# Performance work log

Hardware: AMD Instinct MI355X
Metric: run time of the kernel (lower is better)

## Reference

```python
import jax, jax.numpy as jnp
import numpy as np

DIM = 1024
N_HEADS = 16
B, S = 2, 2048


def setup_inputs() -> dict:
    key = jax.random.key(0)
    ks = jax.random.split(key, 5)
    scale = 1.0 / np.sqrt(DIM)
    x = jax.random.normal(ks[0], (B, S, DIM), dtype=jnp.float32)
    mask = jax.random.randint(ks[1], (B, S), 0, 2, dtype=jnp.int32)
    Wq = jax.random.normal(ks[2], (DIM, DIM), dtype=jnp.float32) * scale
    Wk = jax.random.normal(ks[3], (DIM, DIM), dtype=jnp.float32) * scale
    Wv = jax.random.normal(ks[4], (DIM, DIM), dtype=jnp.float32) * scale
    bq = jnp.zeros((DIM,), jnp.float32)
    bk = jnp.zeros((DIM,), jnp.float32)
    bv = jnp.zeros((DIM,), jnp.float32)
    return {"x": x, "mask": mask, "Wq": Wq, "bq": bq, "Wk": Wk, "bk": bk, "Wv": Wv, "bv": bv}


def reference(x, mask, Wq, bq, Wk, bk, Wv, bv):
    # x: (B,S,D); project to q,k,v then split heads: (B,H,S,Dh)
    H = N_HEADS
    Bn, Sn, D = x.shape
    Dh = D // H

    def heads(t):
        return t.reshape(Bn, Sn, H, Dh).transpose(0, 2, 1, 3)

    q = heads(x @ Wq + bq)
    k = heads(x @ Wk + bk)
    v = heads(x @ Wv + bv)

    scores = jnp.einsum("bhsd,bhtd->bhst", q, k) / jnp.sqrt(jnp.float32(Dh))
    m = mask.astype(jnp.float32)[:, None, None, :]  # (B,1,1,S)
    scores = scores - 10000.0 * (1.0 - m)
    attn = jax.nn.softmax(scores, axis=-1)  # dropout is identity at eval (p=0)
    h = jnp.einsum("bhst,bhtd->bhsd", attn, v)
    return h.transpose(0, 2, 1, 3).reshape(Bn, Sn, D)
```

## Files before the change

### kernel.cpp

```cpp
#include <hip/hip_runtime.h>
#include <math.h>

#define DIMD 1024
#define NH 16
#define DH 64
#define BB 2
#define SS 2048
#define M_TOTAL (BB * SS)

typedef _Float16 half8 __attribute__((ext_vector_type(8)));
typedef _Float16 half4v __attribute__((ext_vector_type(4)));
typedef __fp16 fp16x2 __attribute__((ext_vector_type(2)));
typedef float floatx4 __attribute__((ext_vector_type(4)));
typedef float floatx16 __attribute__((ext_vector_type(16)));

#define QSCALE 0.18033688011112042f

__device__ __forceinline__ void load16_to_lds(const void* g, void* l) {
    __builtin_amdgcn_global_load_lds(
        (const __attribute__((address_space(1))) void*)g,
        (__attribute__((address_space(3))) void*)l, 16, 0, 0);
}

__global__ __launch_bounds__(256) void prep_kernel(
    const float* __restrict__ x,
    const float* __restrict__ Wq, const float* __restrict__ Wk,
    const float* __restrict__ Wv, const int* __restrict__ mask,
    _Float16* __restrict__ xh, _Float16* __restrict__ Wt,
    int* __restrict__ pos, int* __restrict__ nvalid)
{
    __shared__ _Float16 Ls[32][34];
    __shared__ int cnt[32], off[32];
    const int bid = blockIdx.x, tid = threadIdx.x;

    if (bid < 1024) {
#pragma unroll
        for (int j = 0; j < 4; ++j) {
            const int i = j * 262144 + bid * 256 + tid;
            float4 v = ((const float4*)x)[i];
            half4v hv = {(_Float16)v.x, (_Float16)v.y, (_Float16)v.z, (_Float16)v.w};
            *(half4v*)&xh[(size_t)i * 4] = hv;
        }
    } else if (bid < 4096) {
        const int wid = bid - 1024;
        const int z = wid >> 10, rem = wid & 1023;
        const float* W = z == 0 ? Wq : (z == 1 ? Wk : Wv);
        _Float16* o = Wt + (size_t)z * DIMD * DIMD;
        const int k0 = (rem >> 5) * 32, n0 = (rem & 31) * 32;
        const int r = tid >> 3, c4 = (tid & 7) * 4;

        float4 v = *(const float4*)&W[(size_t)(k0 + r) * DIMD + n0 + c4];
        Ls[r][c4 + 0] = (_Float16)v.x;
        Ls[r][c4 + 1] = (_Float16)v.y;
        Ls[r][c4 + 2] = (_Float16)v.z;
        Ls[r][c4 + 3] = (_Float16)v.w;
        __syncthreads();
        half4v h = {Ls[c4 + 0][r], Ls[c4 + 1][r], Ls[c4 + 2][r], Ls[c4 + 3][r]};
        *(half4v*)&o[(size_t)(n0 + r) * DIMD + k0 + c4] = h;
    } else {
        const int b = bid - 4096;
        const int wv = tid >> 6, lane = tid & 63;
        const unsigned long long lanemask = (lane == 63)
            ? 0x7fffffffffffffffull : ((1ull << lane) - 1ull);
        unsigned long long bms[8];
#pragma unroll
        for (int cc = 0; cc < 8; ++cc) {
            const int c = wv * 8 + cc;
            const int mv = mask[b * SS + c * 64 + lane];
            bms[cc] = __ballot(mv != 0);
            if (lane == 0) cnt[c] = __popcll(bms[cc]);
        }
        __syncthreads();
        if (tid == 0) {
            int s = 0;
            for (int c = 0; c < 32; ++c) { off[c] = s; s += cnt[c]; }
            nvalid[b] = s;
        }
        __syncthreads();
#pragma unroll
        for (int cc = 0; cc < 8; ++cc) {
            const int c = wv * 8 + cc;
            const int valid = (int)((bms[cc] >> lane) & 1ull);
            pos[b * SS + c * 64 + lane] =
                valid ? (off[c] + __popcll(bms[cc] & lanemask)) : -1;
        }
    }
}

__global__ __launch_bounds__(256) void proj_gemm(
    const _Float16* __restrict__ xh, const _Float16* __restrict__ Wt,
    const float* __restrict__ bq, const float* __restrict__ bk,
    const float* __restrict__ bv, const int* __restrict__ pos,
    _Float16* __restrict__ Q, _Float16* __restrict__ K, _Float16* __restrict__ Vt)
{
    const int z = blockIdx.z;
    const float* bias = z == 0 ? bq : (z == 1 ? bk : bv);
    const _Float16* Wz = Wt + (size_t)z * DIMD * DIMD;

    const _Float16* Aptr; const _Float16* Bptr; int m0, n0;
    if (z == 2) { Aptr = Wz; Bptr = xh; m0 = blockIdx.y * 128; n0 = blockIdx.x * 128; }
    else        { Aptr = xh; Bptr = Wz; m0 = blockIdx.x * 128; n0 = blockIdx.y * 128; }

    __shared__ _Float16 Ah[2][128 * 32];
    __shared__ _Float16 Bh[2][128 * 32];

    const int tid = threadIdx.x;
    const int wave = tid >> 6, lane = tid & 63;
    const int quad = lane >> 4, l16 = lane & 15;
    const int wm = (wave >> 1) * 64, wn = (wave & 1) * 64;

    floatx4 acc[4][4];
#pragma unroll
    for (int i = 0; i < 4; ++i)
#pragma unroll
        for (int j = 0; j < 4; ++j) acc[i][j] = (floatx4){0.f, 0.f, 0.f, 0.f};

    auto stage = [&](int buf, int k0) {
#pragma unroll
        for (int it = 0; it < 2; ++it) {
            const int u = it * 256 + tid;
            const int row = u >> 2;
            const int gc = (u & 3) ^ ((row >> 1) & 3);
            load16_to_lds(&Aptr[(size_t)(m0 + row) * DIMD + k0 + gc * 8],
                          &Ah[buf][(size_t)(it * 256 + wave * 64) * 8]);
        }
#pragma unroll
        for (int it = 0; it < 2; ++it) {
            const int u = it * 256 + tid;
            const int row = u >> 2;
            const int gc = (u & 3) ^ ((row >> 1) & 3);
            load16_to_lds(&Bptr[(size_t)(n0 + row) * DIMD + k0 + gc * 8],
                          &Bh[buf][(size_t)(it * 256 + wave * 64) * 8]);
        }
    };

    stage(0, 0);
    __syncthreads();

    for (int kt = 0; kt < 32; ++kt) {
        if (kt + 1 < 32) stage((kt + 1) & 1, (kt + 1) * 32);

        const _Float16* A = Ah[kt & 1];
        const _Float16* B = Bh[kt & 1];
        half8 af[4], bf[4];
#pragma unroll
        for (int mt = 0; mt < 4; ++mt) {
            const int row = wm + mt * 16 + l16;
            af[mt] = *(const half8*)&A[row * 32 + ((quad ^ ((row >> 1) & 3)) << 3)];
        }
#pragma unroll
        for (int nt = 0; nt < 4; ++nt) {
            const int row = wn + nt * 16 + l16;
            bf[nt] = *(const half8*)&B[row * 32 + ((quad ^ ((row >> 1) & 3)) << 3)];
        }
#pragma unroll
        for (int mt = 0; mt < 4; ++mt)
#pragma unroll
            for (int nt = 0; nt < 4; ++nt)
                acc[mt][nt] = __builtin_amdgcn_mfma_f32_16x16x32_f16(
                    af[mt], bf[nt], acc[mt][nt], 0, 0, 0);

        __syncthreads();
    }

    if (z < 2) {
        int prr[4][4];
#pragma unroll
        for (int mt = 0; mt < 4; ++mt)
#pragma unroll
            for (int r = 0; r < 4; ++r) {
                const int m = m0 + wm + mt * 16 + quad * 4 + r;
                prr[mt][r] = (z == 0) ? (m & 2047) : pos[m];
            }
#pragma unroll
        for (int nt = 0; nt < 4; ++nt) {
            const int n = n0 + wn + nt * 16 + l16;
            const float bn = bias[n];
            const int h = n >> 6, d = n & 63;
#pragma unroll
            for (int mt = 0; mt < 4; ++mt) {
#pragma unroll
                for (int r = 0; r < 4; ++r) {
                    if (prr[mt][r] < 0) continue;
                    const int m = m0 + wm + mt * 16 + quad * 4 + r;
                    const int b = m >> 11;
                    const _Float16 val = (_Float16)((acc[mt][nt][r] + bn) *
                                                    (z == 0 ? QSCALE : 1.0f));
                    _Float16* dst = (z == 0) ? Q : K;
                    dst[((((size_t)b * NH + h) * SS + prr[mt][r]) << 6) + d] = val;
                }
            }
        }
    } else {
#pragma unroll
        for (int nt = 0; nt < 4; ++nt) {
            const int gs = n0 + wn + nt * 16 + l16;
            const int prn = pos[gs];
            const int b = gs >> 11;
#pragma unroll
            for (int mt = 0; mt < 4; ++mt) {
#pragma unroll
                for (int r = 0; r < 4; ++r) {
                    if (prn < 0) continue;
                    const int drow = m0 + wm + mt * 16 + quad * 4 + r;
                    const int h = drow >> 6, dh = drow & 63;
                    Vt[(((size_t)b * NH + h) * DH + dh) * SS + prn] =
                        (_Float16)(acc[mt][nt][r] + bias[drow]);
                }
            }
        }
    }
}

__global__ __launch_bounds__(256, 2) void attn_kernel(
    const _Float16* __restrict__ Q, const _Float16* __restrict__ K,
    const _Float16* __restrict__ Vt, const int* __restrict__ nvalid,
    float* __restrict__ out)
{
    __shared__ __align__(16) char smem[34816];
    const int bh = blockIdx.y, b = bh >> 4, h = bh & 15;
    const int q0 = blockIdx.x * 128;
    const int tid = threadIdx.x, wave = tid >> 6, lane = tid & 63;
    const int hi = lane >> 5, l31 = lane & 31;

    const _Float16* Qb = Q + (size_t)bh * SS * DH;
    const _Float16* Kb = K + (size_t)bh * SS * DH;
    const _Float16* Vtb = Vt + (size_t)bh * DH * SS;

    const int nv = nvalid[b];
    const int ntiles = (nv + 63) >> 6;

    half8 qf[4];
#pragma unroll
    for (int ks = 0; ks < 4; ++ks)
        qf[ks] = *(const half8*)&Qb[(size_t)(q0 + wave * 32 + l31) * DH
                                    + ks * 16 + hi * 8];

#pragma unroll
    for (int it = 0; it < 2; ++it) {
        const int u = it * 256 + tid;
        const int row = u >> 3, gc = (u & 7) ^ (row & 7);
        load16_to_lds(&Kb[(size_t)row * DH + gc * 8],
                      (_Float16*)smem + (size_t)(it * 256 + wave * 64) * 8);
    }
#pragma unroll
    for (int it = 0; it < 2; ++it) {
        const int u = it * 256 + tid;
        const int row = u >> 3, gc = (u & 7) ^ (row & 7);
        load16_to_lds(&Vtb[(size_t)row * SS + gc * 8],
                      (_Float16*)(smem + 16384) + (size_t)(it * 256 + wave * 64) * 8);
    }
    __syncthreads();

    floatx16 O0, O1;
#pragma unroll
    for (int r = 0; r < 16; ++r) { O0[r] = 0.f; O1[r] = 0.f; }
    float m = -1e30f, l = 0.f;

    for (int i = 0; i < ntiles; ++i) {
        const int buf = i & 1;
        const int t0 = i * 64;

        if (i + 1 < ntiles) {
            const int nb = buf ^ 1, nt0 = t0 + 64;
            _Float16* KsN = (_Float16*)(smem + nb * 8192);
#pragma unroll
            for (int it = 0; it < 2; ++it) {
                const int u = it * 256 + tid;
                const int row = u >> 3, gc = (u & 7) ^ (row & 7);
                load16_to_lds(&Kb[(size_t)(nt0 + row) * DH + gc * 8],
                              KsN + (size_t)(it * 256 + wave * 64) * 8);
            }
            _Float16* VtN = (_Float16*)(smem + 16384 + nb * 8192);
#pragma unroll
            for (int it = 0; it < 2; ++it) {
                const int u = it * 256 + tid;
                const int row = u >> 3, gc = (u & 7) ^ (row & 7);
                load16_to_lds(&Vtb[(size_t)row * SS + nt0 + gc * 8],
                              VtN + (size_t)(it * 256 + wave * 64) * 8);
            }
        }

        const _Float16* KsB = (const _Float16*)(smem + buf * 8192);
        const _Float16* VtB = (const _Float16*)(smem + 16384 + buf * 8192);

        floatx16 S0, S1;
#pragma unroll
        for (int r = 0; r < 16; ++r) { S0[r] = 0.f; S1[r] = 0.f; }
#pragma unroll
        for (int ks = 0; ks < 4; ++ks) {
            const int c = 2 * ks + hi;
            const int r0 = l31, r1 = 32 + l31;
            half8 a0 = *(const half8*)&KsB[r0 * 64 + ((c ^ (r0 & 7)) << 3)];
            half8 a1 = *(const half8*)&KsB[r1 * 64 + ((c ^ (r1 & 7)) << 3)];
            S0 = __builtin_amdgcn_mfma_f32_32x32x16_f16(a0, qf[ks], S0, 0, 0, 0);
            S1 = __builtin_amdgcn_mfma_f32_32x32x16_f16(a1, qf[ks], S1, 0, 0, 0);
        }

        if (t0 + 64 > nv) {
#pragma unroll
            for (int r = 0; r < 16; ++r) {
                const int tr = (r & 3) + 8 * (r >> 2) + 4 * hi;
                S0[r] = (t0 + tr < nv) ? S0[r] : -1e30f;
                S1[r] = (t0 + 32 + tr < nv) ? S1[r] : -1e30f;
            }
        }

        float tmax = -1e30f;
#pragma unroll
        for (int r = 0; r < 16; ++r)
            tmax = fmaxf(tmax, fmaxf(S0[r], S1[r]));
        tmax = fmaxf(tmax, __shfl_xor(tmax, 32));
        const float mn = fmaxf(m, tmax);
        const float alpha = exp2f(m - mn);
        m = mn;

        float p0[16], p1[16];
        float lsum = 0.f;
#pragma unroll
        for (int r = 0; r < 16; ++r) {
            const float e0 = exp2f(S0[r] - m);
            const float e1 = exp2f(S1[r] - m);
            p0[r] = e0; p1[r] = e1;
            lsum += e0 + e1;
        }
        lsum += __shfl_xor(lsum, 32);
        l = l * alpha + lsum;
#pragma unroll
        for (int r = 0; r < 16; ++r) { O0[r] *= alpha; O1[r] *= alpha; }

        unsigned int pk0[8], pk1[8];
#pragma unroll
        for (int j = 0; j < 8; ++j) {
            union { fp16x2 hv; unsigned int u; } cv;
            cv.hv = __builtin_amdgcn_cvt_pkrtz(p0[2 * j], p0[2 * j + 1]);
            pk0[j] = cv.u;
            cv.hv = __builtin_amdgcn_cvt_pkrtz(p1[2 * j], p1[2 * j + 1]);
            pk1[j] = cv.u;
        }

#pragma unroll
        for (int ks = 0; ks < 4; ++ks) {
            const int k1 = ks & 1;
            const unsigned int* pk = (ks < 2) ? pk0 : pk1;
            const unsigned int a0 = pk[4 * k1 + 0], a1 = pk[4 * k1 + 1];
            const unsigned int b0 = pk[4 * k1 + 2], b1 = pk[4 * k1 + 3];
            const unsigned int s0 = hi ? a0 : b0, s1 = hi ? a1 : b1;
            const unsigned int r0v = __shfl_xor(s0, 32);
            const unsigned int r1v = __shfl_xor(s1, 32);
            union { unsigned int u[4]; half8 hv; } bfu;
            bfu.u[0] = hi ? r0v : a0;
            bfu.u[1] = hi ? r1v : a1;
            bfu.u[2] = hi ? b0 : r0v;
            bfu.u[3] = hi ? b1 : r1v;
            const int c = 2 * ks + hi;
            const int rd0 = l31, rd1 = 32 + l31;
            half8 v0 = *(const half8*)&VtB[rd0 * 64 + ((c ^ (rd0 & 7)) << 3)];
            half8 v1 = *(const half8*)&VtB[rd1 * 64 + ((c ^ (rd1 & 7)) << 3)];
            O0 = __builtin_amdgcn_mfma_f32_32x32x16_f16(v0, bfu.hv, O0, 0, 0, 0);
            O1 = __builtin_amdgcn_mfma_f32_32x32x16_f16(v1, bfu.hv, O1, 0, 0, 0);
        }

        __syncthreads();
    }

    const float inv = 1.f / l;
    float* Ob = (float*)smem + wave * (32 * 68);
#pragma unroll
    for (int r = 0; r < 16; ++r) {
        const int dbase = (r & 3) + 8 * (r >> 2) + 4 * hi;
        Ob[l31 * 68 + dbase] = O0[r] * inv;
        Ob[l31 * 68 + 32 + dbase] = O1[r] * inv;
    }
    __syncthreads();

    const int qq = lane >> 1, part = lane & 1;
    float* op = out + ((size_t)(b * SS + q0 + wave * 32 + qq)) * DIMD
              + h * DH + part * 32;
#pragma unroll
    for (int j = 0; j < 8; ++j)
        *(float4*)&op[j * 4] = *(const float4*)&Ob[qq * 68 + part * 32 + j * 4];
}

extern "C" void kernel_launch(void* const* d_in, const int* in_sizes, int n_in,
                              void* d_out, int out_size, void* d_ws, size_t ws_size,
                              hipStream_t stream) {
    const float* x  = (const float*)d_in[0];
    const int* mask = (const int*)d_in[1];
    const float* Wq = (const float*)d_in[2];
    const float* bq = (const float*)d_in[3];
    const float* Wk = (const float*)d_in[4];
    const float* bk = (const float*)d_in[5];
    const float* Wv = (const float*)d_in[6];
    const float* bv = (const float*)d_in[7];
    float* out = (float*)d_out;

    _Float16* xh = (_Float16*)d_ws;
    _Float16* Wt = xh + (size_t)M_TOTAL * DIMD;
    _Float16* Q  = Wt + (size_t)3 * DIMD * DIMD;
    _Float16* K  = Q + (size_t)M_TOTAL * DIMD;
    _Float16* Vt = K + (size_t)M_TOTAL * DIMD;
    int* pos     = (int*)(Vt + (size_t)M_TOTAL * DIMD);
    int* nvalid  = pos + M_TOTAL;

    prep_kernel<<<4098, 256, 0, stream>>>(x, Wq, Wk, Wv, mask, xh, Wt, pos, nvalid);
    proj_gemm<<<dim3(32, 8, 3), 256, 0, stream>>>(
        xh, Wt, bq, bk, bv, pos, Q, K, Vt);
    attn_kernel<<<dim3(SS / 128, BB * NH), 256, 0, stream>>>(Q, K, Vt, nvalid, out);
}
```

Measured before the change: 191.5 us.

## Use single-buffered 64-wide K tiles in projection GEMM with 8-way swizzle

Replaces the double-buffered 32-wide K staging in the QKV projection GEMM with a single buffer holding 64-wide K tiles. The LDS swizzle moves to an XOR over 8 chunks. Each tile now feeds two MFMA sub-steps, which halves the number of barrier-separated iterations. The cost is that global-to-LDS loads no longer overlap compute, since two syncthreads bracket every load phase, so latency hiding now depends on occupancy rather than software pipelining.

```diff
diff --git a/kernel.cpp b/kernel.cpp
--- a/kernel.cpp
+++ b/kernel.cpp
@@ -101,13 +101,14 @@
     if (z == 2) { Aptr = Wz; Bptr = xh; m0 = blockIdx.y * 128; n0 = blockIdx.x * 128; }
     else        { Aptr = xh; Bptr = Wz; m0 = blockIdx.x * 128; n0 = blockIdx.y * 128; }
 
-    __shared__ _Float16 Ah[2][128 * 32];
-    __shared__ _Float16 Bh[2][128 * 32];
+    __shared__ _Float16 Ah[128 * 64];
+    __shared__ _Float16 Bh[128 * 64];
 
     const int tid = threadIdx.x;
     const int wave = tid >> 6, lane = tid & 63;
     const int quad = lane >> 4, l16 = lane & 15;
     const int wm = (wave >> 1) * 64, wn = (wave & 1) * 64;
+    const int sw = l16 & 7;
 
     floatx4 acc[4][4];
 #pragma unroll
@@ -115,52 +116,43 @@
 #pragma unroll
         for (int j = 0; j < 4; ++j) acc[i][j] = (floatx4){0.f, 0.f, 0.f, 0.f};
 
-    auto stage = [&](int buf, int k0) {
-#pragma unroll
-        for (int it = 0; it < 2; ++it) {
+    for (int k0 = 0; k0 < DIMD; k0 += 64) {
+        __syncthreads();
+#pragma unroll
+        for (int it = 0; it < 4; ++it) {
             const int u = it * 256 + tid;
-            const int row = u >> 2;
-            const int gc = (u & 3) ^ ((row >> 1) & 3);
+            const int row = u >> 3;
+            const int gc = (u & 7) ^ (row & 7);
             load16_to_lds(&Aptr[(size_t)(m0 + row) * DIMD + k0 + gc * 8],
-                          &Ah[buf][(size_t)(it * 256 + wave * 64) * 8]);
-        }
-#pragma unroll
-        for (int it = 0; it < 2; ++it) {
+                          &Ah[(size_t)(it * 256 + wave * 64) * 8]);
+        }
+#pragma unroll
+        for (int it = 0; it < 4; ++it) {
             const int u = it * 256 + tid;
-            const int row = u >> 2;
-            const int gc = (u & 3) ^ ((row >> 1) & 3);
+            const int row = u >> 3;
+            const int gc = (u & 7) ^ (row & 7);
             load16_to_lds(&Bptr[(size_t)(n0 + row) * DIMD + k0 + gc * 8],
-                          &Bh[buf][(size_t)(it * 256 + wave * 64) * 8]);
-        }
-    };
-
-    stage(0, 0);
-    __syncthreads();
-
-    for (int kt = 0; kt < 32; ++kt) {
-        if (kt + 1 < 32) stage((kt + 1) & 1, (kt + 1) * 32);
-
-        const _Float16* A = Ah[kt & 1];
-        const _Float16* B = Bh[kt & 1];
-        half8 af[4], bf[4];
-#pragma unroll
-        for (int mt = 0; mt < 4; ++mt) {
-            const int row = wm + mt * 16 + l16;
-            af[mt] = *(const half8*)&A[row * 32 + ((quad ^ ((row >> 1) & 3)) << 3)];
-        }
-#pragma unroll
-        for (int nt = 0; nt < 4; ++nt) {
-            const int row = wn + nt * 16 + l16;
-            bf[nt] = *(const half8*)&B[row * 32 + ((quad ^ ((row >> 1) & 3)) << 3)];
-        }
-#pragma unroll
-        for (int mt = 0; mt < 4; ++mt)
+                          &Bh[(size_t)(it * 256 + wave * 64) * 8]);
+        }
+        __syncthreads();
+
+#pragma unroll
+        for (int kc = 0; kc < 2; ++kc) {
+            const int coff = ((quad + kc * 4) ^ sw) * 8;
+            half8 af[4], bf[4];
+#pragma unroll
+            for (int mt = 0; mt < 4; ++mt)
+                af[mt] = *(const half8*)&Ah[(wm + mt * 16 + l16) * 64 + coff];
 #pragma unroll
             for (int nt = 0; nt < 4; ++nt)
-                acc[mt][nt] = __builtin_amdgcn_mfma_f32_16x16x32_f16(
-                    af[mt], bf[nt], acc[mt][nt], 0, 0, 0);
-
-        __syncthreads();
+                bf[nt] = *(const half8*)&Bh[(wn + nt * 16 + l16) * 64 + coff];
+#pragma unroll
+            for (int mt = 0; mt < 4; ++mt)
+#pragma unroll
+                for (int nt = 0; nt < 4; ++nt)
+                    acc[mt][nt] = __builtin_amdgcn_mfma_f32_16x16x32_f16(
+                        af[mt], bf[nt], acc[mt][nt], 0, 0, 0);
+        }
     }
 
     if (z < 2) {
```

Result: faster. 183.1 us (-4.4%).
